# Optimization experiments

Measured on AMD Instinct MI355X. Metric: run time of the kernel, lower is better.

Reference implementation:

```python
import jax, jax.numpy as jnp
import numpy as np

B, S, H = 2, 1024, 2048          # batch, seq, hidden
NH, HD = 32, 64                  # heads, head_dim
E, M, K = 8, 1024, 2             # experts, moe_dim, top_k
EPS = 1e-5
ROPE_THETA = 10000.0


def setup_inputs() -> dict:
    key = jax.random.key(0)
    ks = jax.random.split(key, 12)
    sc = lambda *sh: 0.02
    return {
        "hidden_states": jax.random.normal(ks[0], (B, S, H), jnp.float32),
        "w_attn_norm": jnp.ones((H,), jnp.float32),
        "Wq": jax.random.normal(ks[1], (H, H), jnp.float32) * 0.02,
        "Wk": jax.random.normal(ks[2], (H, H), jnp.float32) * 0.02,
        "Wv": jax.random.normal(ks[3], (H, H), jnp.float32) * 0.02,
        "Wo": jax.random.normal(ks[4], (H, H), jnp.float32) * 0.02,
        "w_moe_norm": jnp.ones((H,), jnp.float32),
        "Wr": jax.random.normal(ks[5], (H, E), jnp.float32) * 0.02,
        "Wgate": jax.random.normal(ks[6], (E, H, M), jnp.float32) * 0.02,
        "Wup": jax.random.normal(ks[7], (E, H, M), jnp.float32) * 0.02,
        "Wdown": jax.random.normal(ks[8], (E, M, H), jnp.float32) * 0.02,
    }


def _rmsnorm(x, w):
    return x * jax.lax.rsqrt(jnp.mean(x * x, axis=-1, keepdims=True) + EPS) * w


def _rope_cos_sin(seq_len, dtype):
    inv_freq = 1.0 / (ROPE_THETA ** (jnp.arange(0, HD, 2, dtype=jnp.float32) / HD))
    ang = jnp.arange(seq_len, dtype=jnp.float32)[:, None] * inv_freq[None, :]  # [S, HD/2]
    cos = jnp.concatenate([jnp.cos(ang), jnp.cos(ang)], axis=-1).astype(dtype)  # [S, HD]
    sin = jnp.concatenate([jnp.sin(ang), jnp.sin(ang)], axis=-1).astype(dtype)
    return cos, sin


def _rotate_half(x):
    x1, x2 = jnp.split(x, 2, axis=-1)
    return jnp.concatenate([-x2, x1], axis=-1)


def _attention(x, Wq, Wk, Wv, Wo, mask):
    b, s, _ = x.shape
    def heads(t):  # [b,s,H] -> [b,NH,s,HD]
        return t.reshape(b, s, NH, HD).transpose(0, 2, 1, 3)
    q, k, v = heads(x @ Wq), heads(x @ Wk), heads(x @ Wv)
    cos, sin = _rope_cos_sin(s, x.dtype)
    q = q * cos + _rotate_half(q) * sin
    k = k * cos + _rotate_half(k) * sin
    scores = jnp.einsum("bhqd,bhkd->bhqk", q, k) / jnp.sqrt(jnp.asarray(HD, x.dtype))
    scores = scores + mask  # [1,1,s,s] causal
    attn = jax.nn.softmax(scores, axis=-1)
    out = jnp.einsum("bhqk,bhkd->bhqd", attn, v)
    out = out.transpose(0, 2, 1, 3).reshape(b, s, H)
    return out @ Wo


def _moe(x, Wr, Wgate, Wup, Wdown):
    b, s, _ = x.shape
    xf = x.reshape(b * s, H)  # [T, H]
    logits = xf @ Wr  # [T, E]
    probs = jax.nn.softmax(logits, axis=-1)
    topv, topi = jax.lax.top_k(probs, K)  # [T, K]
    topv = topv / jnp.sum(topv, axis=-1, keepdims=True)
    # combine weights [T, E], zero for unselected experts
    cw = jnp.sum(jax.nn.one_hot(topi, E, dtype=xf.dtype) * topv[..., None], axis=1)
    g = jnp.einsum("th,ehm->etm", xf, Wgate)
    u = jnp.einsum("th,ehm->etm", xf, Wup)
    h = jax.nn.silu(g) * u
    expert_out = jnp.einsum("etm,emh->eth", h, Wdown)  # [E, T, H]
    out = jnp.einsum("eth,te->th", expert_out, cw)
    return out.reshape(b, s, H)


def reference(hidden_states, w_attn_norm, Wq, Wk, Wv, Wo, w_moe_norm, Wr, Wgate, Wup, Wdown):
    b, s, _ = hidden_states.shape
    causal = jnp.triu(jnp.full((s, s), -jnp.inf, hidden_states.dtype), k=1)[None, None]
    residual = hidden_states
    x = _rmsnorm(hidden_states, w_attn_norm)
    x = _attention(x, Wq, Wk, Wv, Wo, causal)
    x = x + residual
    residual = x
    y = _rmsnorm(x, w_moe_norm)
    y = _moe(y, Wr, Wgate, Wup, Wdown)
    return y + residual
```

## Files before the change

### kernel.cpp

```cpp
#include <hip/hip_runtime.h>
#include <hip/hip_bf16.h>
#include <cstdint>

typedef unsigned short u16;
typedef __bf16 bf16x4_t __attribute__((ext_vector_type(4)));
typedef __bf16 bf16x8_t __attribute__((ext_vector_type(8)));
typedef float f32x4_t __attribute__((ext_vector_type(4)));
typedef unsigned short us4_t __attribute__((ext_vector_type(4)));
typedef unsigned short us8_t __attribute__((ext_vector_type(8)));

#define BATCH 2
#define SEQ 1024
#define HID 2048
#define NHEAD 32
#define NEXP 8
#define MDIM 1024
#define T_TOK (BATCH*SEQ)


__device__ __forceinline__ void gload16(const void* g, void* l){
  __builtin_amdgcn_global_load_lds((__attribute__((address_space(1))) void*)(uintptr_t)g,
                                   (__attribute__((address_space(3))) void*)l, 16, 0, 0);
}

__device__ __forceinline__ bf16x8_t ldfsw64(const u16* base, int row, int colbyte){
  const char* p = (const char*)base + row*64;
  int sw = (row & 3) << 4;
  bf16x4_t a = *(const bf16x4_t*)(p + (colbyte ^ sw));
  bf16x4_t b = *(const bf16x4_t*)(p + ((colbyte + 32) ^ sw));
  return __builtin_shufflevector(a, b, 0,1,2,3,4,5,6,7);
}

__device__ __forceinline__ f32x4_t mfma16(bf16x8_t a, bf16x8_t b, f32x4_t c){
  return __builtin_amdgcn_mfma_f32_16x16x32_bf16(a, b, c, 0, 0, 0);
}

__device__ __forceinline__ u16 f2b(float f){
  __hip_bfloat16 h = __float2bfloat16(f);
  return __builtin_bit_cast(u16, h);
}
__device__ __forceinline__ float b2f(u16 b){
  return __builtin_bit_cast(float, (unsigned int)b << 16);
}
__device__ __forceinline__ void split3v(float v, u16& b1, u16& b2, u16& b3){
  b1 = f2b(v); float f1 = b2f(b1);
  float r1 = v - f1;
  b2 = f2b(r1); float f2 = b2f(b2);
  b3 = f2b(r1 - f2);
}



__global__ __launch_bounds__(256)
void convT_fl(const float* __restrict__ in, u16* __restrict__ out, int R, int C)
{
  __shared__ float t[64][65];
  const int KB = C >> 5;
  int bz = blockIdx.z;
  const float* ip = in + (size_t)bz * R * C;
  u16* op = out + (size_t)bz * R * C;
  int r0 = blockIdx.y*64, c0 = blockIdx.x*64;
  int tid = threadIdx.x;
  int lr = tid >> 4;
  int lc = (tid & 15) * 4;
  #pragma unroll
  for (int i = 0; i < 4; i++){
    int r = lr + i*16;
    float4 v = *(const float4*)&ip[(size_t)(r0 + r) * R + c0 + lc];
    t[r][lc] = v.x; t[r][lc+1] = v.y; t[r][lc+2] = v.z; t[r][lc+3] = v.w;
  }
  __syncthreads();
  if (tid < 128){
    int n_l = tid & 63;
    int kb2 = tid >> 6;
    int gn = c0 + n_l;
    int rb = gn >> 7, sub = (gn >> 4) & 7, frn = gn & 15;
    int kb = (r0 >> 5) + kb2;
    size_t fo = (((size_t)(rb*KB + kb)*8 + sub)*64 + frn*4) * 8;
    #pragma unroll
    for (int fg = 0; fg < 4; fg++){
      us8_t w;
      #pragma unroll
      for (int j = 0; j < 4; j++){
        w[j]   = f2b(t[kb2*32 + fg*4 + j][n_l]);
        w[j+4] = f2b(t[kb2*32 + fg*4 + 16 + j][n_l]);
      }
      *(us8_t*)&op[fo + fg*8] = w;
    }
  }
}


__global__ __launch_bounds__(256)
void convT3(const float* __restrict__ in, u16* __restrict__ o1, u16* __restrict__ o2,
            u16* __restrict__ o3)
{
  __shared__ float t[64][65];
  int r0 = blockIdx.y*64, c0 = blockIdx.x*64;
  int tid = threadIdx.x;
  int lr = tid >> 4;
  int lc = (tid & 15) * 4;
  #pragma unroll
  for (int i = 0; i < 4; i++){
    int r = lr + i*16;
    float4 v = *(const float4*)&in[(size_t)(r0 + r) * HID + c0 + lc];
    t[r][lc] = v.x; t[r][lc+1] = v.y; t[r][lc+2] = v.z; t[r][lc+3] = v.w;
  }
  __syncthreads();
  if (tid < 128){
    int n  = tid & 63;
    int kb2 = tid >> 6;
    int gn = c0 + n;
    int nb = gn >> 7, sub = (gn >> 4) & 7, fr = gn & 15;
    int kb = (r0 >> 5) + kb2;
    size_t fo = (((size_t)(nb*64 + kb)*8 + sub)*64 + fr*4) * 8;
    #pragma unroll
    for (int fg = 0; fg < 4; fg++){
      us8_t w1, w2, w3;
      #pragma unroll
      for (int j = 0; j < 4; j++){
        u16 b1, b2, b3;
        split3v(t[kb2*32 + fg*4 + j][n], b1, b2, b3);
        w1[j] = b1; w2[j] = b2; w3[j] = b3;
        split3v(t[kb2*32 + fg*4 + 16 + j][n], b1, b2, b3);
        w1[j+4] = b1; w2[j+4] = b2; w3[j+4] = b3;
      }
      *(us8_t*)&o1[fo + fg*8] = w1;
      *(us8_t*)&o2[fo + fg*8] = w2;
      *(us8_t*)&o3[fo + fg*8] = w3;
    }
  }
}


__global__ __launch_bounds__(256)
void rmsnorm3_k(const float* __restrict__ x, const float* __restrict__ w,
                u16* __restrict__ o1, u16* __restrict__ o2, u16* __restrict__ o3)
{
  int row = blockIdx.x;
  const float* xr = x + (size_t)row * HID;
  int tid = threadIdx.x;
  int kb = tid >> 2, fg = tid & 3;
  int kbase = kb*32 + fg*4;
  float4 a = *(const float4*)(xr + kbase);
  float4 b = *(const float4*)(xr + kbase + 16);
  float ss = a.x*a.x + a.y*a.y + a.z*a.z + a.w*a.w
           + b.x*b.x + b.y*b.y + b.z*b.z + b.w*b.w;
  #pragma unroll
  for (int off = 32; off; off >>= 1) ss += __shfl_down(ss, off);
  __shared__ float red[4];
  if ((tid & 63) == 0) red[tid >> 6] = ss;
  __syncthreads();
  float tot = red[0] + red[1] + red[2] + red[3];
  float rs = (float)(1.0 / sqrt((double)tot * (1.0/2048.0) + 1e-5));
  float4 wa = *(const float4*)(w + kbase);
  float4 wb = *(const float4*)(w + kbase + 16);
  float o[8];
  o[0]=a.x*rs*wa.x; o[1]=a.y*rs*wa.y; o[2]=a.z*rs*wa.z; o[3]=a.w*rs*wa.w;
  o[4]=b.x*rs*wb.x; o[5]=b.y*rs*wb.y; o[6]=b.z*rs*wb.z; o[7]=b.w*rs*wb.w;
  us8_t w1, w2, w3;
  #pragma unroll
  for (int j = 0; j < 8; j++){
    u16 b1, b2, b3; split3v(o[j], b1, b2, b3);
    w1[j] = b1; w2[j] = b2; w3[j] = b3;
  }
  int rb = row >> 7, sub = (row >> 4) & 7, fr = row & 15;
  size_t fo = (((size_t)(rb*64 + kb)*8 + sub)*64 + fr*4 + fg) * 8;
  *(us8_t*)&o1[fo] = w1; *(us8_t*)&o2[fo] = w2; *(us8_t*)&o3[fo] = w3;
}


__global__ __launch_bounds__(256)
void rmsnorm_k(const float* __restrict__ x, const float* __restrict__ w,
               u16* __restrict__ ob, float* __restrict__ of, float* __restrict__ oi)
{
  int row = blockIdx.x;
  const float* xr = x + (size_t)row * HID;
  int base = threadIdx.x * 8;
  float4 a = *(const float4*)(xr + base);
  float4 b = *(const float4*)(xr + base + 4);
  float ss = a.x*a.x + a.y*a.y + a.z*a.z + a.w*a.w
           + b.x*b.x + b.y*b.y + b.z*b.z + b.w*b.w;
  #pragma unroll
  for (int off = 32; off; off >>= 1) ss += __shfl_down(ss, off);
  __shared__ float red[4];
  if ((threadIdx.x & 63) == 0) red[threadIdx.x >> 6] = ss;
  __syncthreads();
  float tot = red[0] + red[1] + red[2] + red[3];
  float rs = (float)(1.0 / sqrt((double)tot * (1.0/2048.0) + 1e-5));
  float4 wa = *(const float4*)(w + base);
  float4 wb = *(const float4*)(w + base + 4);
  float o[8];
  o[0]=a.x*rs*wa.x; o[1]=a.y*rs*wa.y; o[2]=a.z*rs*wa.z; o[3]=a.w*rs*wa.w;
  o[4]=b.x*rs*wb.x; o[5]=b.y*rs*wb.y; o[6]=b.z*rs*wb.z; o[7]=b.w*rs*wb.w;
  us4_t p0, p1;
  p0.x=f2b(o[0]); p0.y=f2b(o[1]); p0.z=f2b(o[2]); p0.w=f2b(o[3]);
  p1.x=f2b(o[4]); p1.y=f2b(o[5]); p1.z=f2b(o[6]); p1.w=f2b(o[7]);
  *(us4_t*)&ob[(size_t)row*HID + base] = p0;
  *(us4_t*)&ob[(size_t)row*HID + base + 4] = p1;
  float* orow = of + (size_t)row*HID + base;
  *(float4*)orow = make_float4(o[0],o[1],o[2],o[3]);
  *(float4*)(orow+4) = make_float4(o[4],o[5],o[6],o[7]);
  float* irow = oi + (size_t)row*HID + base;
  *(float4*)irow = a;
  *(float4*)(irow+4) = b;
}


__global__ void rope_table_k(float* ct, float* st){
  int i = blockIdx.x*256 + threadIdx.x;
  int s = i >> 5, j = i & 31;
  double invf = exp(-(double)j / 32.0 * log(10000.0));
  double ang = (double)s * invf;
  ct[i] = (float)cos(ang);
  st[i] = (float)sin(ang);
}


__global__ __launch_bounds__(256, 2)
void gemm_qkv(const u16* __restrict__ A1, const u16* __restrict__ A2, const u16* __restrict__ A3,
              const u16* __restrict__ Wq1, const u16* __restrict__ Wq2, const u16* __restrict__ Wq3,
              const u16* __restrict__ Wk1, const u16* __restrict__ Wk2, const u16* __restrict__ Wk3,
              const u16* __restrict__ Wv1, const u16* __restrict__ Wv2, const u16* __restrict__ Wv3,
              u16* __restrict__ oq1, u16* __restrict__ oq2, u16* __restrict__ oq3,
              u16* __restrict__ ok1, u16* __restrict__ ok2, u16* __restrict__ ok3,
              u16* __restrict__ vt1, u16* __restrict__ vt2, u16* __restrict__ vt3,
              const float* __restrict__ ct, const float* __restrict__ st)
{
  __shared__ u16 As[3][128*32];
  __shared__ u16 Bs[3][128*32];
  const int flat = blockIdx.x + 16*blockIdx.y + 256*blockIdx.z;
  const int logical = (flat & 7) * 96 + (flat >> 3);
  const int z  = logical >> 8;
  const int bm = ((logical >> 4) & 15) * 128;
  const int bn = (logical & 15) * 128;
  const int tid = threadIdx.x;
  const int lane = tid & 63;
  const int wave = tid >> 6;
  const int wr = wave >> 1, wc = wave & 1;
  const int fr = lane & 15, fg = lane >> 4;

  f32x4_t acc[4][4] = {};

  const u16* Ap[3] = {A1, A2, A3};
  const u16* Bp[3];
  if (z == 0)      { Bp[0] = Wq1; Bp[1] = Wq2; Bp[2] = Wq3; }
  else if (z == 1) { Bp[0] = Wk1; Bp[1] = Wk2; Bp[2] = Wk3; }
  else             { Bp[0] = Wv1; Bp[1] = Wv2; Bp[2] = Wv3; }
  const u16* gA[3]; const u16* gB[3];
  #pragma unroll
  for (int t = 0; t < 3; t++){
    gA[t] = Ap[t] + (size_t)(bm >> 7) * 262144 + tid*8;
    gB[t] = Bp[t] + (size_t)(bn >> 7) * 262144 + tid*8;
  }

  for (int kb = 0; kb < 64; kb++){
    const size_t o = (size_t)kb * 4096;
    #pragma unroll
    for (int t = 0; t < 3; t++){
      gload16(gA[t] + o,        &As[t][tid*8]);
      gload16(gA[t] + o + 2048, &As[t][2048 + tid*8]);
      gload16(gB[t] + o,        &Bs[t][tid*8]);
      gload16(gB[t] + o + 2048, &Bs[t][2048 + tid*8]);
    }
    __syncthreads();
    bf16x8_t bfv[3][4];
    #pragma unroll
    for (int t = 0; t < 3; t++)
      #pragma unroll
      for (int ni = 0; ni < 4; ni++)
        bfv[t][ni] = *(const bf16x8_t*)&Bs[t][(((wc*4 + ni)*64) + fr*4 + fg)*8];
    #pragma unroll
    for (int mi = 0; mi < 4; mi++){
      const int ao = (((wr*4 + mi)*64) + fr*4 + fg)*8;
      bf16x8_t a1 = *(const bf16x8_t*)&As[0][ao];
      bf16x8_t a2 = *(const bf16x8_t*)&As[1][ao];
      bf16x8_t a3 = *(const bf16x8_t*)&As[2][ao];
      #pragma unroll
      for (int ni = 0; ni < 4; ni++){
        f32x4_t c = acc[mi][ni];
        c = mfma16(a3, bfv[0][ni], c);
        c = mfma16(a2, bfv[1][ni], c);
        c = mfma16(a1, bfv[2][ni], c);
        c = mfma16(a2, bfv[0][ni], c);
        c = mfma16(a1, bfv[1][ni], c);
        c = mfma16(a1, bfv[0][ni], c);
        acc[mi][ni] = c;
      }
    }
    __syncthreads();
  }

  if (z < 2){
    u16* O1 = z ? ok1 : oq1;
    u16* O2 = z ? ok2 : oq2;
    u16* O3 = z ? ok3 : oq3;
    const int h = (bn + wc*64) >> 6;
    #pragma unroll
    for (int mi = 0; mi < 4; mi++)
      #pragma unroll
      for (int r = 0; r < 4; r++){
        int row = bm + wr*64 + mi*16 + fg*4 + r;
        int s = row & (SEQ-1);
        int b = row >> 10;
        int tok = row & 1023;
        int tb = tok >> 4;
        int frk = fg*4 + r;
        size_t sb = (size_t)(b*NHEAD + h) * 65536;
        #pragma unroll
        for (int ni = 0; ni < 2; ni++){
          int dlo = ni*16 + fr;
          float c  = ct[s*32 + dlo];
          float sn = st[s*32 + dlo];
          float xl = acc[mi][ni][r], xh = acc[mi][ni+2][r];
          float ol = xl*c - xh*sn;
          float oh = xh*c + xl*sn;
          size_t a0 = sb + ((size_t)(tb*2 + 0)*64 + frk*4 + (fr>>2))*8 + ni*4 + (fr&3);
          size_t a1 = sb + ((size_t)(tb*2 + 1)*64 + frk*4 + (fr>>2))*8 + ni*4 + (fr&3);
          u16 b1, b2, b3;
          split3v(ol, b1, b2, b3); O1[a0] = b1; O2[a0] = b2; O3[a0] = b3;
          split3v(oh, b1, b2, b3); O1[a1] = b1; O2[a1] = b2; O3[a1] = b3;
        }
      }
  } else {
    const int h = (bn + wc*64) >> 6;
    const int b = bm >> 10;
    const size_t sb = (size_t)(b*NHEAD + h) * 65536;
    const int tokb = (bm & 1023) + wr*64;
    #pragma unroll
    for (int mi = 0; mi < 4; mi++){
      const int kbv = (tokb + mi*16) >> 5;
      const int el = (mi & 1) * 4;
      #pragma unroll
      for (int ni = 0; ni < 4; ni++){
        us4_t v1, v2, v3;
        #pragma unroll
        for (int r = 0; r < 4; r++){
          u16 b1, b2, b3; split3v(acc[mi][ni][r], b1, b2, b3);
          v1[r] = b1; v2[r] = b2; v3[r] = b3;
        }
        size_t a = sb + ((size_t)(kbv*4 + ni)*64 + fr*4 + fg)*8 + el;
        *(us4_t*)&vt1[a] = v1; *(us4_t*)&vt2[a] = v2; *(us4_t*)&vt3[a] = v3;
      }
    }
  }
}


__global__ __launch_bounds__(256, 2)
void gemm_o(const u16* __restrict__ A1, const u16* __restrict__ A2, const u16* __restrict__ A3,
            const u16* __restrict__ B1, const u16* __restrict__ B2, const u16* __restrict__ B3,
            float* __restrict__ Cf, const float* __restrict__ Res)
{
  __shared__ u16 As[3][128*32];
  __shared__ u16 Bs[3][64*32];
  const int flat = blockIdx.x + 32*blockIdx.y;
  const int logical = (flat & 7) * 64 + (flat >> 3);
  const int bn = (logical & 31) * 64;
  const int bm = (logical >> 5) * 128;
  const int tid = threadIdx.x;
  const int lane = tid & 63;
  const int wave = tid >> 6;
  const int wr = wave >> 1, wc = wave & 1;
  const int fr = lane & 15, fg = lane >> 4;

  f32x4_t acc[4][2] = {};

  const u16* Ap[3] = {A1, A2, A3};
  const u16* Bp[3] = {B1, B2, B3};
  const u16* gA[3]; const u16* gB[3];
  const int sb0 = (bn >> 4) & 7;
  #pragma unroll
  for (int t = 0; t < 3; t++){
    gA[t] = Ap[t] + (size_t)(bm >> 7) * 262144 + tid*8;
    gB[t] = Bp[t] + (size_t)(bn >> 7) * 262144 + sb0*512 + tid*8;
  }

  for (int kb = 0; kb < 64; kb++){
    const size_t o = (size_t)kb * 4096;
    #pragma unroll
    for (int t = 0; t < 3; t++){
      gload16(gA[t] + o,        &As[t][tid*8]);
      gload16(gA[t] + o + 2048, &As[t][2048 + tid*8]);
      gload16(gB[t] + o,        &Bs[t][tid*8]);
    }
    __syncthreads();
    bf16x8_t bfv[3][2];
    #pragma unroll
    for (int t = 0; t < 3; t++)
      #pragma unroll
      for (int nj = 0; nj < 2; nj++)
        bfv[t][nj] = *(const bf16x8_t*)&Bs[t][(((wc*2 + nj)*64) + fr*4 + fg)*8];
    #pragma unroll
    for (int mi = 0; mi < 4; mi++){
      const int ao = (((wr*4 + mi)*64) + fr*4 + fg)*8;
      bf16x8_t a1 = *(const bf16x8_t*)&As[0][ao];
      bf16x8_t a2 = *(const bf16x8_t*)&As[1][ao];
      bf16x8_t a3 = *(const bf16x8_t*)&As[2][ao];
      #pragma unroll
      for (int nj = 0; nj < 2; nj++){
        f32x4_t c = acc[mi][nj];
        c = mfma16(a3, bfv[0][nj], c);
        c = mfma16(a2, bfv[1][nj], c);
        c = mfma16(a1, bfv[2][nj], c);
        c = mfma16(a2, bfv[0][nj], c);
        c = mfma16(a1, bfv[1][nj], c);
        c = mfma16(a1, bfv[0][nj], c);
        acc[mi][nj] = c;
      }
    }
    __syncthreads();
  }

  #pragma unroll
  for (int mi = 0; mi < 4; mi++)
    #pragma unroll
    for (int nj = 0; nj < 2; nj++)
      #pragma unroll
      for (int r = 0; r < 4; r++){
        int row = bm + wr*64 + mi*16 + fg*4 + r;
        int col = bn + wc*32 + nj*16 + fr;
        size_t idx = (size_t)row * HID + col;
        Cf[idx] = acc[mi][nj][r] + Res[idx];
      }
}


__global__ __launch_bounds__(256)
void fattn3_k(const u16* __restrict__ q1, const u16* __restrict__ q2, const u16* __restrict__ q3,
              const u16* __restrict__ k1, const u16* __restrict__ k2, const u16* __restrict__ k3,
              const u16* __restrict__ v1, const u16* __restrict__ v2, const u16* __restrict__ v3,
              u16* __restrict__ ao1, u16* __restrict__ ao2, u16* __restrict__ ao3)
{
  __shared__ u16 Ks[3][4096];
  __shared__ u16 Vs[3][4096];
  __shared__ u16 Ps[2][4][1024];
  const int flat = blockIdx.x + 64*blockIdx.y;
  const int logical = (flat & 7) * 128 + (flat >> 3);
  const int bh = logical >> 4, qt = logical & 15;
  const int b = bh >> 5, h = bh & 31;
  const int tid = threadIdx.x, lane = tid & 63, wave = tid >> 6;
  const int fr = lane & 15, fg = lane >> 4;
  const size_t hslab = (size_t)bh * 65536;

  bf16x8_t aq[3][2];
  {
    size_t qo = hslab + (size_t)(qt*4 + wave)*1024 + (size_t)(fr*4 + fg)*8;
    aq[0][0] = *(const bf16x8_t*)&q1[qo]; aq[0][1] = *(const bf16x8_t*)&q1[qo + 512];
    aq[1][0] = *(const bf16x8_t*)&q2[qo]; aq[1][1] = *(const bf16x8_t*)&q2[qo + 512];
    aq[2][0] = *(const bf16x8_t*)&q3[qo]; aq[2][1] = *(const bf16x8_t*)&q3[qo + 512];
  }

  f32x4_t oacc[4] = {};
  float m_r[4], l_r[4];
  #pragma unroll
  for (int r = 0; r < 4; r++){ m_r[r] = -1e30f; l_r[r] = 0.f; }

  const u16* kp[3] = { k1 + hslab, k2 + hslab, k3 + hslab };
  const u16* vp[3] = { v1 + hslab, v2 + hslab, v3 + hslab };

  for (int kt = 0; kt <= qt; kt++){
    const size_t o = (size_t)kt * 4096;
    #pragma unroll
    for (int t = 0; t < 3; t++){
      gload16(kp[t] + o + tid*8,        &Ks[t][tid*8]);
      gload16(kp[t] + o + 2048 + tid*8, &Ks[t][2048 + tid*8]);
      gload16(vp[t] + o + tid*8,        &Vs[t][tid*8]);
      gload16(vp[t] + o + 2048 + tid*8, &Vs[t][2048 + tid*8]);
    }
    __syncthreads();

    f32x4_t sc[4] = {};
    #pragma unroll
    for (int nf = 0; nf < 4; nf++)
      #pragma unroll
      for (int ks = 0; ks < 2; ks++){
        const int ko = ((nf*2 + ks)*64 + fr*4 + fg)*8;
        bf16x8_t bk0 = *(const bf16x8_t*)&Ks[0][ko];
        bf16x8_t bk1 = *(const bf16x8_t*)&Ks[1][ko];
        bf16x8_t bk2 = *(const bf16x8_t*)&Ks[2][ko];
        sc[nf] = mfma16(aq[2][ks], bk0, sc[nf]);
        sc[nf] = mfma16(aq[1][ks], bk1, sc[nf]);
        sc[nf] = mfma16(aq[0][ks], bk2, sc[nf]);
        sc[nf] = mfma16(aq[1][ks], bk0, sc[nf]);
        sc[nf] = mfma16(aq[0][ks], bk1, sc[nf]);
        sc[nf] = mfma16(aq[0][ks], bk0, sc[nf]);
      }

    float nm[4] = {-1e30f,-1e30f,-1e30f,-1e30f};
    #pragma unroll
    for (int nf = 0; nf < 4; nf++)
      #pragma unroll
      for (int r = 0; r < 4; r++){
        float v = sc[nf][r] * 0.125f;
        if (kt == qt && nf*16 + fr > wave*16 + fg*4 + r) v = -1e30f;
        sc[nf][r] = v;
        nm[r] = fmaxf(nm[r], v);
      }
    #pragma unroll
    for (int r = 0; r < 4; r++)
      #pragma unroll
      for (int msk = 8; msk; msk >>= 1) nm[r] = fmaxf(nm[r], __shfl_xor(nm[r], msk));

    #pragma unroll
    for (int r = 0; r < 4; r++){
      float mn = fmaxf(m_r[r], nm[r]);
      float f = __expf(m_r[r] - mn);
      m_r[r] = mn;
      float rsum = 0.f;
      #pragma unroll
      for (int nf = 0; nf < 4; nf++){
        float pv = __expf(sc[nf][r] - mn);
        sc[nf][r] = pv;
        rsum += pv;
      }
      #pragma unroll
      for (int msk = 8; msk; msk >>= 1) rsum += __shfl_xor(rsum, msk);
      l_r[r] = l_r[r]*f + rsum;
      #pragma unroll
      for (int df = 0; df < 4; df++) oacc[df][r] *= f;
    }

    #pragma unroll
    for (int nf = 0; nf < 4; nf++)
      #pragma unroll
      for (int r = 0; r < 4; r++){
        float pv = sc[nf][r];
        u16 b1 = f2b(pv);
        float f1 = b2f(b1);
        u16 b2 = f2b(pv - f1);
        int pa = ((nf>>1)*64 + (fg*4 + r)*4 + (fr>>2))*8 + (nf&1)*4 + (fr&3);
        Ps[0][wave][pa] = b1;
        Ps[1][wave][pa] = b2;
      }

    #pragma unroll
    for (int ks = 0; ks < 2; ks++){
      bf16x8_t pa0 = *(const bf16x8_t*)&Ps[0][wave][(ks*64 + fr*4 + fg)*8];
      bf16x8_t pa1 = *(const bf16x8_t*)&Ps[1][wave][(ks*64 + fr*4 + fg)*8];
      #pragma unroll
      for (int df = 0; df < 4; df++){
        const int vo = ((ks*4 + df)*64 + fr*4 + fg)*8;
        bf16x8_t bv0 = *(const bf16x8_t*)&Vs[0][vo];
        bf16x8_t bv1 = *(const bf16x8_t*)&Vs[1][vo];
        bf16x8_t bv2 = *(const bf16x8_t*)&Vs[2][vo];
        oacc[df] = mfma16(pa0, bv2, oacc[df]);
        oacc[df] = mfma16(pa1, bv1, oacc[df]);
        oacc[df] = mfma16(pa1, bv0, oacc[df]);
        oacc[df] = mfma16(pa0, bv1, oacc[df]);
        oacc[df] = mfma16(pa0, bv0, oacc[df]);
      }
    }
    __syncthreads();
  }

  #pragma unroll
  for (int r = 0; r < 4; r++){
    float inv = 1.f / l_r[r];
    int orow = b*SEQ + qt*64 + wave*16 + fg*4 + r;
    int rb = orow >> 7, sub = (orow >> 4) & 7, frA = orow & 15;
    #pragma unroll
    for (int df = 0; df < 4; df++){
      float val = oacc[df][r] * inv;
      int kb = h*2 + (df >> 1);
      size_t addr = ((((size_t)rb*64 + kb)*8 + sub)*64 + frA*4 + (fr>>2))*8 + (df&1)*4 + (fr&3);
      u16 b1, b2, b3; split3v(val, b1, b2, b3);
      ao1[addr] = b1; ao2[addr] = b2; ao3[addr] = b3;
    }
  }
}


__global__ __launch_bounds__(64)
void router_scatter_k(const float* __restrict__ yn, const float* __restrict__ Wr,
                      int* __restrict__ tok_list, float* __restrict__ w_list,
                      int* __restrict__ cur){
  int row = blockIdx.x;
  int lane = threadIdx.x;
  const float* xr = yn + (size_t)row * HID;
  double acc[8] = {};
  for (int j = lane; j < HID; j += 64){
    double xv = (double)xr[j];
    const float* wr = Wr + (size_t)j*8;
    float4 w0 = *(const float4*)wr;
    float4 w1 = *(const float4*)(wr + 4);
    acc[0] += xv*w0.x; acc[1] += xv*w0.y; acc[2] += xv*w0.z; acc[3] += xv*w0.w;
    acc[4] += xv*w1.x; acc[5] += xv*w1.y; acc[6] += xv*w1.z; acc[7] += xv*w1.w;
  }
  #pragma unroll
  for (int e = 0; e < 8; e++)
    #pragma unroll
    for (int off = 32; off; off >>= 1) acc[e] += __shfl_down(acc[e], off);
  if (lane == 0){
    double mx = acc[0];
    #pragma unroll
    for (int e = 1; e < 8; e++) mx = fmax(mx, acc[e]);
    double p[8];
    #pragma unroll
    for (int e = 0; e < 8; e++) p[e] = exp(acc[e] - mx);
    int i1 = 0;
    #pragma unroll
    for (int e = 1; e < 8; e++) if (p[e] > p[i1]) i1 = e;
    int i2 = (i1 == 0) ? 1 : 0;
    #pragma unroll
    for (int e = 0; e < 8; e++) if (e != i1 && p[e] > p[i2]) i2 = e;
    double s2 = p[i1] + p[i2];
    int pos1 = atomicAdd(&cur[i1], 1);
    tok_list[i1*T_TOK + pos1] = row;
    w_list[i1*T_TOK + pos1] = (float)(p[i1] / s2);
    int pos2 = atomicAdd(&cur[i2], 1);
    tok_list[i2*T_TOK + pos2] = row;
    w_list[i2*T_TOK + pos2] = (float)(p[i2] / s2);
  }
}

__global__ __launch_bounds__(128)
void pad_k(const int* __restrict__ cur, int* __restrict__ tok_list,
           float* __restrict__ w_list, int* __restrict__ cnt_pad){
  int e = blockIdx.x;
  int c = cur[e];
  int cp = (c + 127) & ~127;
  for (int i = c + threadIdx.x; i < cp; i += 128){
    tok_list[e*T_TOK + i] = 0;
    w_list[e*T_TOK + i] = 0.f;
  }
  if (threadIdx.x == 0) cnt_pad[e] = cp;
}


__global__ __launch_bounds__(256, 2)
void gemm_gateup_sp(const u16* __restrict__ A, const u16* __restrict__ WgT, const u16* __restrict__ WuT,
                    const int* __restrict__ tok_list, const float* __restrict__ w_list,
                    const int* __restrict__ cnt_pad, u16* __restrict__ Hb)
{
  const int e = blockIdx.z;
  const int bm = blockIdx.y * 128;
  if (bm >= cnt_pad[e]) return;
  __shared__ u16 As[128*32];
  __shared__ u16 Bg[64*32];
  __shared__ u16 Bu[64*32];
  const int tid = threadIdx.x;
  const int lane = tid & 63;
  const int wave = tid >> 6;
  const int wr = wave >> 1, wc = wave & 1;
  const int fr = lane & 15, fg = lane >> 4;
  const int bn = blockIdx.x * 64;

  f32x4_t ag[4][2] = {}, au[4][2] = {};

  const int srow = tid >> 2, skb = (tid & 3) ^ (srow & 3);
  const int tok0 = tok_list[e*T_TOK + bm + srow];
  const int tok1 = tok_list[e*T_TOK + bm + srow + 64];
  const u16* ga0 = A + (size_t)tok0 * HID + skb * 8;
  const u16* ga1 = A + (size_t)tok1 * HID + skb * 8;
  const int sub0 = (bn >> 4) & 7;
  const u16* gg = WgT + (size_t)e*MDIM*HID + ((size_t)(bn>>7)*512 + sub0)*512 + tid*8;
  const u16* gu = WuT + (size_t)e*MDIM*HID + ((size_t)(bn>>7)*512 + sub0)*512 + tid*8;

  for (int kb = 0; kb < 64; kb++){
    gload16(ga0 + kb*32, &As[tid*8]);
    gload16(ga1 + kb*32, &As[2048 + tid*8]);
    gload16(gg + (size_t)kb*4096, &Bg[tid*8]);
    gload16(gu + (size_t)kb*4096, &Bu[tid*8]);
    __syncthreads();
    bf16x8_t af[4], bg[2], bu[2];
    #pragma unroll
    for (int i = 0; i < 4; i++) af[i] = ldfsw64(As, wr*64 + i*16 + fr, fg*8);
    #pragma unroll
    for (int j = 0; j < 2; j++){
      bg[j] = *(const bf16x8_t*)&Bg[((wc*2 + j)*64 + fr*4 + fg)*8];
      bu[j] = *(const bf16x8_t*)&Bu[((wc*2 + j)*64 + fr*4 + fg)*8];
    }
    #pragma unroll
    for (int mi = 0; mi < 4; mi++)
      #pragma unroll
      for (int nj = 0; nj < 2; nj++){
        ag[mi][nj] = mfma16(af[mi], bg[nj], ag[mi][nj]);
        au[mi][nj] = mfma16(af[mi], bu[nj], au[mi][nj]);
      }
    __syncthreads();
  }

  #pragma unroll
  for (int mi = 0; mi < 4; mi++)
    #pragma unroll
    for (int nj = 0; nj < 2; nj++)
      #pragma unroll
      for (int r = 0; r < 4; r++){
        int pos = bm + wr*64 + mi*16 + fg*4 + r;
        int col = bn + wc*32 + nj*16 + fr;
        float g = ag[mi][nj][r], u = au[mi][nj][r];
        float h = g / (1.0f + __expf(-g)) * u * w_list[e*T_TOK + pos];
        Hb[((size_t)e*T_TOK + pos)*MDIM + col] = f2b(h);
      }
}


__global__ __launch_bounds__(256, 2)
void gemm_down_sp(const u16* __restrict__ Hb, const u16* __restrict__ WdT,
                  const int* __restrict__ tok_list, const int* __restrict__ cnt_pad,
                  float* __restrict__ Out)
{
  const int e = blockIdx.z;
  const int bm = blockIdx.y * 128;
  if (bm >= cnt_pad[e]) return;
  __shared__ u16 As[128*32];
  __shared__ u16 Bs[128*32];
  const int tid = threadIdx.x;
  const int lane = tid & 63;
  const int wave = tid >> 6;
  const int wr = wave >> 1, wc = wave & 1;
  const int fr = lane & 15, fg = lane >> 4;
  const int bn = blockIdx.x * 128;
  const int srow = tid >> 2, skb = (tid & 3) ^ (srow & 3);

  f32x4_t acc[4][4] = {};

  const u16* A  = Hb  + (size_t)e * T_TOK * MDIM;
  const u16* ga0 = A + (size_t)(bm + srow) * MDIM + skb * 8;
  const u16* gB = WdT + (size_t)e*HID*MDIM + (size_t)(bn>>7)*131072 + tid*8;
  for (int kb = 0; kb < 32; kb++){
    gload16(ga0 + kb*32, &As[tid*8]);
    gload16(ga0 + (size_t)64*MDIM + kb*32, &As[2048 + tid*8]);
    gload16(gB + (size_t)kb*4096,        &Bs[tid*8]);
    gload16(gB + (size_t)kb*4096 + 2048, &Bs[2048 + tid*8]);
    __syncthreads();
    bf16x8_t af[4], bfv[4];
    #pragma unroll
    for (int i = 0; i < 4; i++) af[i]  = ldfsw64(As, wr*64 + i*16 + fr, fg*8);
    #pragma unroll
    for (int i = 0; i < 4; i++) bfv[i] = *(const bf16x8_t*)&Bs[((wc*4 + i)*64 + fr*4 + fg)*8];
    #pragma unroll
    for (int mi = 0; mi < 4; mi++)
      #pragma unroll
      for (int ni = 0; ni < 4; ni++)
        acc[mi][ni] = mfma16(af[mi], bfv[ni], acc[mi][ni]);
    __syncthreads();
  }

  #pragma unroll
  for (int mi = 0; mi < 4; mi++)
    #pragma unroll
    for (int r = 0; r < 4; r++){
      int pos = bm + wr*64 + mi*16 + fg*4 + r;
      int tok = tok_list[e*T_TOK + pos];
      #pragma unroll
      for (int ni = 0; ni < 4; ni++){
        int col = bn + wc*64 + ni*16 + fr;
        atomicAdd(&Out[(size_t)tok * HID + col], acc[mi][ni][r]);
      }
    }
}


extern "C" void kernel_launch(void* const* d_in, const int* in_sizes, int n_in,
                              void* d_out, int out_size, void* d_ws, size_t ws_size,
                              hipStream_t stream)
{
  const float* hs     = (const float*)d_in[0];
  const float* w_attn = (const float*)d_in[1];
  const float* Wq = (const float*)d_in[2];
  const float* Wk = (const float*)d_in[3];
  const float* Wv = (const float*)d_in[4];
  const float* Wo = (const float*)d_in[5];
  const float* w_moe = (const float*)d_in[6];
  const float* Wr = (const float*)d_in[7];
  const float* Wg = (const float*)d_in[8];
  const float* Wu = (const float*)d_in[9];
  const float* Wd = (const float*)d_in[10];
  float* out = (float*)d_out;
  (void)in_sizes; (void)n_in; (void)out_size; (void)ws_size;

  char* ws = (char*)d_ws;
  const size_t MB = 1024*1024;
  char* R0 = ws;
  char* R1 = ws + 96*MB;
  char* R2 = ws + 120*MB;
  char* R3 = ws + 144*MB;
  char* R5 = ws + 168*MB;
  char* R6 = ws + 192*MB;
  char* RS = ws + 216*MB;

  const size_t WSLB = (size_t)HID*HID;
  u16* W0 = (u16*)R0;
  u16 *Wq1 = W0,          *Wq2 = W0 + WSLB,    *Wq3 = W0 + 2*WSLB;
  u16 *Wk1 = W0 + 3*WSLB, *Wk2 = W0 + 4*WSLB,  *Wk3 = W0 + 5*WSLB;
  u16 *Wv1 = W0 + 6*WSLB, *Wv2 = W0 + 7*WSLB,  *Wv3 = W0 + 8*WSLB;
  u16 *Wo1 = W0 + 9*WSLB, *Wo2 = W0 + 10*WSLB, *Wo3 = W0 + 11*WSLB;
  const size_t TSLB = (size_t)T_TOK*HID;
  u16 *xn1 = (u16*)R1, *xn2 = (u16*)R1 + TSLB, *xn3 = (u16*)R1 + 2*TSLB;
  u16 *q1  = (u16*)R2, *q2  = (u16*)R2 + TSLB, *q3  = (u16*)R2 + 2*TSLB;
  u16 *k1  = (u16*)R3, *k2  = (u16*)R3 + TSLB, *k3  = (u16*)R3 + 2*TSLB;
  u16 *ao1 = (u16*)R5, *ao2 = (u16*)R5 + TSLB, *ao3 = (u16*)R5 + 2*TSLB;
  u16 *vt1 = (u16*)R6, *vt2 = (u16*)R6 + TSLB, *vt3 = (u16*)R6 + 2*TSLB;
  float* x1  = (float*)R6;
  u16* WgT = (u16*)R0;
  u16* WuT = (u16*)R0 + (size_t)NEXP*MDIM*HID;
  u16* WdT = (u16*)R0 + 2*(size_t)NEXP*MDIM*HID;
  u16* ynb = (u16*)R1;
  float* yn = (float*)(R1 + 8*MB);
  u16* hb  = (u16*)R2;
  int*   tok_list = (int*)RS;
  float* w_list   = (float*)(RS + 64*1024);
  int*   cur      = (int*)(RS + 128*1024);
  int*   cnt_pad  = (int*)(RS + 132*1024);
  float* ct   = (float*)(RS + 256*1024);
  float* stab = (float*)(RS + 384*1024);

  dim3 blk256(256), gMoE(16,16,8);

  rope_table_k<<<dim3(SEQ*32/256), blk256, 0, stream>>>(ct, stab);
  convT3<<<dim3(HID/64, HID/64), blk256, 0, stream>>>(Wq, Wq1, Wq2, Wq3);
  convT3<<<dim3(HID/64, HID/64), blk256, 0, stream>>>(Wk, Wk1, Wk2, Wk3);
  convT3<<<dim3(HID/64, HID/64), blk256, 0, stream>>>(Wv, Wv1, Wv2, Wv3);
  convT3<<<dim3(HID/64, HID/64), blk256, 0, stream>>>(Wo, Wo1, Wo2, Wo3);

  rmsnorm3_k<<<dim3(T_TOK), blk256, 0, stream>>>(hs, w_attn, xn1, xn2, xn3);

  gemm_qkv<<<dim3(16,16,3), blk256, 0, stream>>>(xn1,xn2,xn3,
      Wq1,Wq2,Wq3, Wk1,Wk2,Wk3, Wv1,Wv2,Wv3,
      q1,q2,q3, k1,k2,k3, vt1,vt2,vt3, ct, stab);

  fattn3_k<<<dim3(64, 16), blk256, 0, stream>>>(q1,q2,q3, k1,k2,k3,
      vt1,vt2,vt3, ao1,ao2,ao3);

  gemm_o<<<dim3(32,16), blk256, 0, stream>>>(ao1,ao2,ao3, Wo1,Wo2,Wo3, x1, hs);

  convT_fl<<<dim3(MDIM/64, HID/64, NEXP), blk256, 0, stream>>>(Wg, WgT, MDIM, HID);
  convT_fl<<<dim3(MDIM/64, HID/64, NEXP), blk256, 0, stream>>>(Wu, WuT, MDIM, HID);
  convT_fl<<<dim3(HID/64, MDIM/64, NEXP), blk256, 0, stream>>>(Wd, WdT, HID, MDIM);

  rmsnorm_k<<<dim3(T_TOK), blk256, 0, stream>>>(x1, w_moe, ynb, yn, out);

  hipMemsetAsync(cur, 0, NEXP*sizeof(int), stream);
  router_scatter_k<<<dim3(T_TOK), dim3(64), 0, stream>>>(yn, Wr, tok_list, w_list, cur);
  pad_k<<<dim3(NEXP), dim3(128), 0, stream>>>(cur, tok_list, w_list, cnt_pad);

  gemm_gateup_sp<<<gMoE, blk256, 0, stream>>>(ynb, WgT, WuT, tok_list, w_list, cnt_pad, hb);
  gemm_down_sp<<<gMoE, blk256, 0, stream>>>(hb, WdT, tok_list, cnt_pad, out);
}
```

Baseline: 855.0 us.

## Widen QKV GEMM tile to 128x256 and drop attention block swizzle

The QKV GEMM block tile grows from 128x128 to 128x256. Each workgroup now loads two B panels and each wave computes 4x8 MFMA fragments, which halves the A-panel reloads and raises MFMA work per LDS read. The epilogue is rewritten to map the wider tile onto two heads per wave. This roughly doubles accumulator registers and raises LDS use, so occupancy may fall. The flash-attention kernel also drops its XCD-aware block-index swizzle and uses blockIdx directly, which changes L2 locality across chiplets.

```diff
diff --git a/kernel.cpp b/kernel.cpp
--- a/kernel.cpp
+++ b/kernel.cpp
@@ -227,64 +227,69 @@
               u16* __restrict__ vt1, u16* __restrict__ vt2, u16* __restrict__ vt3,
               const float* __restrict__ ct, const float* __restrict__ st)
 {
-  __shared__ u16 As[3][128*32];
-  __shared__ u16 Bs[3][128*32];
-  const int flat = blockIdx.x + 16*blockIdx.y + 256*blockIdx.z;
-  const int logical = (flat & 7) * 96 + (flat >> 3);
-  const int z  = logical >> 8;
-  const int bm = ((logical >> 4) & 15) * 128;
-  const int bn = (logical & 15) * 128;
+  __shared__ u16 As[3][4096];
+  __shared__ u16 Bs[3][2][4096];
+  const int flat = blockIdx.x + 8*blockIdx.y + 128*blockIdx.z;
+  const int logical = (flat & 7) * 48 + (flat >> 3);
+  const int z    = logical >> 7;
+  const int rr   = logical & 127;
+  const int bm_i = rr >> 3;
+  const int bn_i = rr & 7;
+  const int bm = bm_i * 128;
   const int tid = threadIdx.x;
   const int lane = tid & 63;
   const int wave = tid >> 6;
   const int wr = wave >> 1, wc = wave & 1;
   const int fr = lane & 15, fg = lane >> 4;
 
-  f32x4_t acc[4][4] = {};
+  f32x4_t acc[4][8] = {};
 
   const u16* Ap[3] = {A1, A2, A3};
   const u16* Bp[3];
   if (z == 0)      { Bp[0] = Wq1; Bp[1] = Wq2; Bp[2] = Wq3; }
   else if (z == 1) { Bp[0] = Wk1; Bp[1] = Wk2; Bp[2] = Wk3; }
   else             { Bp[0] = Wv1; Bp[1] = Wv2; Bp[2] = Wv3; }
-  const u16* gA[3]; const u16* gB[3];
+  const u16* gA[3]; const u16* gB0[3]; const u16* gB1[3];
   #pragma unroll
   for (int t = 0; t < 3; t++){
-    gA[t] = Ap[t] + (size_t)(bm >> 7) * 262144 + tid*8;
-    gB[t] = Bp[t] + (size_t)(bn >> 7) * 262144 + tid*8;
+    gA[t]  = Ap[t] + (size_t)bm_i * 262144 + tid*8;
+    gB0[t] = Bp[t] + (size_t)(2*bn_i)     * 262144 + tid*8;
+    gB1[t] = Bp[t] + (size_t)(2*bn_i + 1) * 262144 + tid*8;
   }
 
   for (int kb = 0; kb < 64; kb++){
     const size_t o = (size_t)kb * 4096;
     #pragma unroll
     for (int t = 0; t < 3; t++){
-      gload16(gA[t] + o,        &As[t][tid*8]);
-      gload16(gA[t] + o + 2048, &As[t][2048 + tid*8]);
-      gload16(gB[t] + o,        &Bs[t][tid*8]);
-      gload16(gB[t] + o + 2048, &Bs[t][2048 + tid*8]);
-    }
-    __syncthreads();
-    bf16x8_t bfv[3][4];
+      gload16(gA[t]  + o,        &As[t][tid*8]);
+      gload16(gA[t]  + o + 2048, &As[t][2048 + tid*8]);
+      gload16(gB0[t] + o,        &Bs[t][0][tid*8]);
+      gload16(gB0[t] + o + 2048, &Bs[t][0][2048 + tid*8]);
+      gload16(gB1[t] + o,        &Bs[t][1][tid*8]);
+      gload16(gB1[t] + o + 2048, &Bs[t][1][2048 + tid*8]);
+    }
+    __syncthreads();
+    bf16x8_t af[3][4];
     #pragma unroll
     for (int t = 0; t < 3; t++)
       #pragma unroll
-      for (int ni = 0; ni < 4; ni++)
-        bfv[t][ni] = *(const bf16x8_t*)&Bs[t][(((wc*4 + ni)*64) + fr*4 + fg)*8];
-    #pragma unroll
-    for (int mi = 0; mi < 4; mi++){
-      const int ao = (((wr*4 + mi)*64) + fr*4 + fg)*8;
-      bf16x8_t a1 = *(const bf16x8_t*)&As[0][ao];
-      bf16x8_t a2 = *(const bf16x8_t*)&As[1][ao];
-      bf16x8_t a3 = *(const bf16x8_t*)&As[2][ao];
-      #pragma unroll
-      for (int ni = 0; ni < 4; ni++){
+      for (int mi = 0; mi < 4; mi++)
+        af[t][mi] = *(const bf16x8_t*)&As[t][(((wr*4 + mi)*64) + fr*4 + fg)*8];
+    #pragma unroll
+    for (int ni = 0; ni < 8; ni++){
+      const int bo = (ni*64 + fr*4 + fg)*8;
+      bf16x8_t b1 = *(const bf16x8_t*)&Bs[0][wc][bo];
+      bf16x8_t b2 = *(const bf16x8_t*)&Bs[1][wc][bo];
+      bf16x8_t b3 = *(const bf16x8_t*)&Bs[2][wc][bo];
+      #pragma unroll
+      for (int mi = 0; mi < 4; mi++){
         f32x4_t c = acc[mi][ni];
-        c = mfma16(a3, bfv[0][ni], c);
-        c = mfma16(a2, bfv[1][ni], c);
-        c = mfma16(a1, bfv[2][ni], c);
-        c = mfma16(a2, bfv[0][ni], c);
-        c = mfma16(a1, bfv[1][ni], c);
-        c = mfma16(a1, bfv[0][ni], c);
+        c = mfma16(af[2][mi], b1, c);
+        c = mfma16(af[1][mi], b2, c);
+        c = mfma16(af[0][mi], b3, c);
+        c = mfma16(af[1][mi], b1, c);
+        c = mfma16(af[0][mi], b2, c);
+        c = mfma16(af[0][mi], b1, c);
         acc[mi][ni] = c;
       }
     }
@@ -295,7 +300,6 @@
     u16* O1 = z ? ok1 : oq1;
     u16* O2 = z ? ok2 : oq2;
     u16* O3 = z ? ok3 : oq3;
-    const int h = (bn + wc*64) >> 6;
     #pragma unroll
     for (int mi = 0; mi < 4; mi++)
       #pragma unroll
@@ -306,40 +310,46 @@
         int tok = row & 1023;
         int tb = tok >> 4;
         int frk = fg*4 + r;
-        size_t sb = (size_t)(b*NHEAD + h) * 65536;
         #pragma unroll
-        for (int ni = 0; ni < 2; ni++){
-          int dlo = ni*16 + fr;
-          float c  = ct[s*32 + dlo];
-          float sn = st[s*32 + dlo];
-          float xl = acc[mi][ni][r], xh = acc[mi][ni+2][r];
-          float ol = xl*c - xh*sn;
-          float oh = xh*c + xl*sn;
-          size_t a0 = sb + ((size_t)(tb*2 + 0)*64 + frk*4 + (fr>>2))*8 + ni*4 + (fr&3);
-          size_t a1 = sb + ((size_t)(tb*2 + 1)*64 + frk*4 + (fr>>2))*8 + ni*4 + (fr&3);
-          u16 b1, b2, b3;
-          split3v(ol, b1, b2, b3); O1[a0] = b1; O2[a0] = b2; O3[a0] = b3;
-          split3v(oh, b1, b2, b3); O1[a1] = b1; O2[a1] = b2; O3[a1] = b3;
+        for (int hh = 0; hh < 2; hh++){
+          int h = bn_i*4 + wc*2 + hh;
+          size_t sb = (size_t)(b*NHEAD + h) * 65536;
+          #pragma unroll
+          for (int nip = 0; nip < 2; nip++){
+            int nl = hh*4 + nip, nh = nl + 2;
+            int dlo = nip*16 + fr;
+            float c  = ct[s*32 + dlo];
+            float sn = st[s*32 + dlo];
+            float xl = acc[mi][nl][r], xh = acc[mi][nh][r];
+            float ol = xl*c - xh*sn;
+            float oh = xh*c + xl*sn;
+            size_t a0 = sb + ((size_t)(tb*2 + 0)*64 + frk*4 + (fr>>2))*8 + nip*4 + (fr&3);
+            size_t a1 = sb + ((size_t)(tb*2 + 1)*64 + frk*4 + (fr>>2))*8 + nip*4 + (fr&3);
+            u16 b1, b2, b3;
+            split3v(ol, b1, b2, b3); O1[a0] = b1; O2[a0] = b2; O3[a0] = b3;
+            split3v(oh, b1, b2, b3); O1[a1] = b1; O2[a1] = b2; O3[a1] = b3;
+          }
         }
       }
   } else {
-    const int h = (bn + wc*64) >> 6;
     const int b = bm >> 10;
-    const size_t sb = (size_t)(b*NHEAD + h) * 65536;
     const int tokb = (bm & 1023) + wr*64;
     #pragma unroll
     for (int mi = 0; mi < 4; mi++){
       const int kbv = (tokb + mi*16) >> 5;
       const int el = (mi & 1) * 4;
       #pragma unroll
-      for (int ni = 0; ni < 4; ni++){
+      for (int ni = 0; ni < 8; ni++){
+        const int hh = ni >> 2, db = ni & 3;
+        const int h = bn_i*4 + wc*2 + hh;
+        const size_t sb = (size_t)(b*NHEAD + h) * 65536;
         us4_t v1, v2, v3;
         #pragma unroll
         for (int r = 0; r < 4; r++){
           u16 b1, b2, b3; split3v(acc[mi][ni][r], b1, b2, b3);
           v1[r] = b1; v2[r] = b2; v3[r] = b3;
         }
-        size_t a = sb + ((size_t)(kbv*4 + ni)*64 + fr*4 + fg)*8 + el;
+        size_t a = sb + ((size_t)(kbv*4 + db)*64 + fr*4 + fg)*8 + el;
         *(us4_t*)&vt1[a] = v1; *(us4_t*)&vt2[a] = v2; *(us4_t*)&vt3[a] = v3;
       }
     }
@@ -435,9 +445,7 @@
   __shared__ u16 Ks[3][4096];
   __shared__ u16 Vs[3][4096];
   __shared__ u16 Ps[2][4][1024];
-  const int flat = blockIdx.x + 64*blockIdx.y;
-  const int logical = (flat & 7) * 128 + (flat >> 3);
-  const int bh = logical >> 4, qt = logical & 15;
+  const int bh = blockIdx.x, qt = blockIdx.y;
   const int b = bh >> 5, h = bh & 31;
   const int tid = threadIdx.x, lane = tid & 63, wave = tid >> 6;
   const int fr = lane & 15, fg = lane >> 4;
@@ -817,7 +825,7 @@
 
   rmsnorm3_k<<<dim3(T_TOK), blk256, 0, stream>>>(hs, w_attn, xn1, xn2, xn3);
 
-  gemm_qkv<<<dim3(16,16,3), blk256, 0, stream>>>(xn1,xn2,xn3,
+  gemm_qkv<<<dim3(8,16,3), blk256, 0, stream>>>(xn1,xn2,xn3,
       Wq1,Wq2,Wq3, Wk1,Wk2,Wk3, Wv1,Wv2,Wv3,
       q1,q2,q3, k1,k2,k3, vt1,vt2,vt3, ct, stab);
 
```

New measurement: 878.7 us. 2.8% more time.
